# Kernel optimization log

Measured on AMD Instinct MI355X. Metric: run time of the kernel, lower is better.

The kernel has to match this reference:

```python
import jax, jax.numpy as jnp
import numpy as np

B, S, E, H, L = 4, 512, 768, 12, 12
D = E // H
FF = 4 * E
EPS = 1e-5
SCALE = jnp.float32(768.0 ** 0.5)  # emb_size ** (1/2), applied AFTER softmax per source


def setup_inputs() -> dict:
    key = jax.random.key(0)
    ks = jax.random.split(key, 18)
    std = 0.02
    n = lambda k, shp: (jax.random.normal(k, shp, jnp.float32) * std)
    return {
        "x": jax.random.normal(ks[0], (B, S, E), jnp.float32),
        "Wqkv": n(ks[1], (L, E, 3 * E)),
        "bqkv": n(ks[2], (L, 3 * E)),
        "Wp": n(ks[3], (L, E, E)),
        "bp": n(ks[4], (L, E)),
        "W1": n(ks[5], (L, E, FF)),
        "b1": n(ks[6], (L, FF)),
        "W2": n(ks[7], (L, FF, E)),
        "b2": n(ks[8], (L, E)),
        "ln1_g": jnp.ones((L, E), jnp.float32), "ln1_b": jnp.zeros((L, E), jnp.float32),
        "ln2_g": jnp.ones((L, E), jnp.float32), "ln2_b": jnp.zeros((L, E), jnp.float32),
        "ln3_g": jnp.ones((L, E), jnp.float32), "ln3_b": jnp.zeros((L, E), jnp.float32),
        "ln4_g": jnp.ones((L, E), jnp.float32), "ln4_b": jnp.zeros((L, E), jnp.float32),
    }


def _ln(x, g, b):
    m = jnp.mean(x, axis=-1, keepdims=True)
    v = jnp.mean(jnp.square(x - m), axis=-1, keepdims=True)
    return (x - m) * jax.lax.rsqrt(v + EPS) * g + b


def _block(x, p):
    Wqkv, bqkv, Wp, bp, W1, b1, W2, b2, g1, be1, g2, be2, g3, be3, g4, be4 = p
    # --- attention branch ---
    h = _ln(x, g1, be1)
    qkv = h @ Wqkv + bqkv                      # [B,S,3E]
    qkv = qkv.reshape(B, S, H, D, 3)           # qkv is innermost factor in source rearrange
    q = jnp.transpose(qkv[..., 0], (0, 2, 1, 3))  # [B,H,S,D]
    k = jnp.transpose(qkv[..., 1], (0, 2, 1, 3))
    v = jnp.transpose(qkv[..., 2], (0, 2, 1, 3))
    energy = jnp.einsum('bhqd,bhkd->bhqk', q, k)
    att = jax.nn.softmax(energy, axis=-1) / SCALE  # NOTE: scaling AFTER softmax (faithful)
    o = jnp.einsum('bhqk,bhkd->bhqd', att, v)
    o = jnp.transpose(o, (0, 2, 1, 3)).reshape(B, S, E)
    o = o @ Wp + bp
    r1 = _ln(o, g2, be2) + x                   # first ResidualAdd (final LN inside branch)
    # --- feed-forward branch ---
    f = _ln(r1, g3, be3)
    f = jax.nn.gelu(f @ W1 + b1, approximate=False)
    f = f @ W2 + b2
    r2 = _ln(f, g4, be4) + r1                  # second ResidualAdd
    return x + r2                              # outer residual: x = x + block(x)


def reference(x, Wqkv, bqkv, Wp, bp, W1, b1, W2, b2,
              ln1_g, ln1_b, ln2_g, ln2_b, ln3_g, ln3_b, ln4_g, ln4_b):
    params = (Wqkv, bqkv, Wp, bp, W1, b1, W2, b2,
              ln1_g, ln1_b, ln2_g, ln2_b, ln3_g, ln3_b, ln4_g, ln4_b)
    out, _ = jax.lax.scan(lambda c, p: (_block(c, p), None), x, params)
    return out
```

## Files before the change

kernel.cpp:

```cpp
#include <hip/hip_runtime.h>
#include <hip/hip_bf16.h>
#include <stdint.h>

#define LAYERS 12
#define M_ROWS 2048
#define E_DIM 768
#define FF_DIM 3072
#define QKV_DIM 2304
#define SCALE_INV 0.036084391824351615f

typedef __hip_bfloat16 bf16;
typedef __attribute__((ext_vector_type(8))) __bf16 bf16x8;
typedef __attribute__((ext_vector_type(4))) float f32x4;

__device__ __forceinline__ float bf2f(bf16 v) { return __bfloat162float(v); }
__device__ __forceinline__ bf16 f2bf(float v) { return __float2bfloat16(v); }

__device__ __forceinline__ float gelu_f(float x) {
  return 0.5f * x * (1.0f + erff(x * 0.70710678118654752f));
}

__global__ __launch_bounds__(256) void transpose_k(
    const float* __restrict__ w0, const float* __restrict__ w1,
    const float* __restrict__ w2, const float* __restrict__ w3,
    bf16* __restrict__ t0, bf16* __restrict__ t1,
    bf16* __restrict__ t2, bf16* __restrict__ t3)
{
  __shared__ float T[32][33];
  int bid = blockIdx.x;
  const float* src; bf16* dst; int K, N, tile;
  if (bid < 1728)      { src = w0; dst = t0; K = 768;  N = 2304; tile = bid; }
  else if (bid < 2304) { src = w1; dst = t1; K = 768;  N = 768;  tile = bid - 1728; }
  else if (bid < 4608) { src = w2; dst = t2; K = 768;  N = 3072; tile = bid - 2304; }
  else                 { src = w3; dst = t3; K = 3072; N = 768;  tile = bid - 4608; }
  int tilesN = N >> 5;
  int tk = tile / tilesN;
  int tn = tile - tk * tilesN;
  int tx = threadIdx.x & 31, ty = threadIdx.x >> 5;
  int k0 = tk << 5, n0 = tn << 5;
#pragma unroll
  for (int i = 0; i < 4; i++)
    T[ty + i * 8][tx] = src[(size_t)(k0 + ty + i * 8) * N + n0 + tx];
  __syncthreads();
#pragma unroll
  for (int i = 0; i < 4; i++)
    dst[(size_t)(n0 + ty + i * 8) * K + k0 + tx] = f2bf(T[tx][ty + i * 8]);
}

template<int OUT_BF16, int NADD>
__global__ __launch_bounds__(256) void ln_k(
    const float* in, const float* gamma, const float* beta,
    const float* add0, const float* add1, void* outp)
{
  int row = blockIdx.x, tid = threadIdx.x;
  const float* x = in + (size_t)row * 768;
  float v[3]; float s = 0.f, sq = 0.f;
#pragma unroll
  for (int j = 0; j < 3; j++) {
    v[j] = x[tid + j * 256];
    s += v[j]; sq += v[j] * v[j];
  }
#pragma unroll
  for (int off = 32; off; off >>= 1) {
    s += __shfl_xor(s, off);
    sq += __shfl_xor(sq, off);
  }
  __shared__ float red[8];
  int wv = tid >> 6;
  if ((tid & 63) == 0) { red[wv] = s; red[4 + wv] = sq; }
  __syncthreads();
  s  = red[0] + red[1] + red[2] + red[3];
  sq = red[4] + red[5] + red[6] + red[7];
  float mean = s * (1.0f / 768.0f);
  float var  = sq * (1.0f / 768.0f) - mean * mean;
  float rstd = rsqrtf(var + 1e-5f);
#pragma unroll
  for (int j = 0; j < 3; j++) {
    int c = tid + j * 256;
    float val = (v[j] - mean) * rstd * gamma[c] + beta[c];
    if (NADD >= 1) val += add0[(size_t)row * 768 + c];
    if (NADD >= 2) val += add1[(size_t)row * 768 + c];
    if (OUT_BF16) ((bf16*)outp)[(size_t)row * 768 + c] = f2bf(val);
    else          ((float*)outp)[(size_t)row * 768 + c] = val;
  }
}

template<int OUT_MODE>
__global__ __launch_bounds__(256) void gemm_k(
    const bf16* __restrict__ A, const bf16* __restrict__ BT,
    const float* __restrict__ bias, void* __restrict__ Cout,
    bf16* __restrict__ qo, bf16* __restrict__ ko, bf16* __restrict__ vo,
    int N, int K)
{
  __shared__ __align__(16) bf16 Als[64 * 32];
  __shared__ __align__(16) bf16 Bls[64 * 32];
  int tid = threadIdx.x;
  int lane = tid & 63, wave = tid >> 6;
  int wm = (wave >> 1) * 32, wn = (wave & 1) * 32;
  int m0 = (blockIdx.x & 31) << 6;
  int n0 = (blockIdx.x >> 5) << 6;
  const bf16* Ap = A + (size_t)m0 * K;
  const bf16* Bp = BT + (size_t)n0 * K;
  int sr = tid >> 2;
  int sc = (tid & 3) * 8;
  f32x4 acc[2][2] = {};
  for (int k0 = 0; k0 < K; k0 += 32) {
    uint4 av = *(const uint4*)(Ap + (size_t)sr * K + k0 + sc);
    uint4 bv = *(const uint4*)(Bp + (size_t)sr * K + k0 + sc);
    __syncthreads();
    *(uint4*)&Als[tid * 8] = av;
    *(uint4*)&Bls[tid * 8] = bv;
    __syncthreads();
    int ko8 = (lane >> 4) * 8;
    bf16x8 af[2], bfr[2];
#pragma unroll
    for (int i = 0; i < 2; i++)
      af[i] = *(const bf16x8*)&Als[(wm + i * 16 + (lane & 15)) * 32 + ko8];
#pragma unroll
    for (int j = 0; j < 2; j++)
      bfr[j] = *(const bf16x8*)&Bls[(wn + j * 16 + (lane & 15)) * 32 + ko8];
#pragma unroll
    for (int i = 0; i < 2; i++)
#pragma unroll
      for (int j = 0; j < 2; j++)
        acc[i][j] = __builtin_amdgcn_mfma_f32_16x16x32_bf16(af[i], bfr[j], acc[i][j], 0, 0, 0);
  }
#pragma unroll
  for (int i = 0; i < 2; i++) {
    int mbase = m0 + wm + i * 16 + ((lane >> 4) << 2);
#pragma unroll
    for (int j = 0; j < 2; j++) {
      int n = n0 + wn + j * 16 + (lane & 15);
      float bvs = bias[n];
      if (OUT_MODE == 3) {
        int h = n / 192;
        int rm = n - h * 192;
        int d = rm / 3;
        int t = rm - d * 3;
#pragma unroll
        for (int rg = 0; rg < 4; rg++) {
          int m = mbase + rg;
          float val = acc[i][j][rg] + bvs;
          int b = m >> 9, sIdx = m & 511;
          int bh = b * 12 + h;
          if (t == 2)
            vo[(size_t)((bh << 6) + d) * 512 + sIdx] = f2bf(val);
          else {
            bf16* dsts = (t == 0) ? qo : ko;
            dsts[(size_t)((bh << 9) + sIdx) * 64 + d] = f2bf(val);
          }
        }
      } else {
#pragma unroll
        for (int rg = 0; rg < 4; rg++) {
          int m = mbase + rg;
          float val = acc[i][j][rg] + bvs;
          if (OUT_MODE == 0)      ((float*)Cout)[(size_t)m * N + n] = val;
          else if (OUT_MODE == 1) ((bf16*)Cout)[(size_t)m * N + n] = f2bf(val);
          else                    ((bf16*)Cout)[(size_t)m * N + n] = f2bf(gelu_f(val));
        }
      }
    }
  }
}

#define PSTR 80
__global__ __launch_bounds__(256) void attn_k(
    const bf16* __restrict__ q, const bf16* __restrict__ k,
    const bf16* __restrict__ vT, bf16* __restrict__ o)
{
  __shared__ __align__(16) bf16 Kls[64 * 64];
  __shared__ __align__(16) bf16 Vls[64 * 64];
  __shared__ __align__(16) bf16 Pls[4][16 * PSTR];
  int tid = threadIdx.x;
  int lane = tid & 63, w = tid >> 6;
  int l15 = lane & 15, l4 = lane >> 4;
  int qt = blockIdx.x & 7;
  int bh = blockIdx.x >> 3;
  size_t base = (size_t)bh * 32768;

  const bf16* qrowp = q + base + (size_t)(qt * 64 + w * 16 + l15) * 64 + l4 * 8;
  bf16x8 qf0 = *(const bf16x8*)qrowp;
  bf16x8 qf1 = *(const bf16x8*)(qrowp + 32);

  float mrow[4] = {-1e30f, -1e30f, -1e30f, -1e30f};
  float lsum[4] = {0.f, 0.f, 0.f, 0.f};
  f32x4 Oacc[4] = {};
  const f32x4 zed = {0.f, 0.f, 0.f, 0.f};
  bf16* pw = &Pls[w][0];

  for (int kt = 0; kt < 8; kt++) {
    __syncthreads();
#pragma unroll
    for (int rep = 0; rep < 2; rep++) {
      int c = tid + rep * 256;
      int row = c >> 3, col8 = (c & 7) * 8;
      *(uint4*)&Kls[row * 64 + col8] =
          *(const uint4*)(k + base + (size_t)(kt * 64 + row) * 64 + col8);
      *(uint4*)&Vls[row * 64 + col8] =
          *(const uint4*)(vT + base + (size_t)row * 512 + kt * 64 + col8);
    }
    __syncthreads();
    f32x4 e[4];
#pragma unroll
    for (int jt = 0; jt < 4; jt++) {
      bf16x8 kf0 = *(const bf16x8*)&Kls[(jt * 16 + l15) * 64 + l4 * 8];
      bf16x8 kf1 = *(const bf16x8*)&Kls[(jt * 16 + l15) * 64 + l4 * 8 + 32];
      e[jt] = __builtin_amdgcn_mfma_f32_16x16x32_bf16(qf0, kf0, zed, 0, 0, 0);
      e[jt] = __builtin_amdgcn_mfma_f32_16x16x32_bf16(qf1, kf1, e[jt], 0, 0, 0);
    }
    float al[4];
#pragma unroll
    for (int rg = 0; rg < 4; rg++) {
      float mn = fmaxf(fmaxf(e[0][rg], e[1][rg]), fmaxf(e[2][rg], e[3][rg]));
#pragma unroll
      for (int off = 1; off < 16; off <<= 1) mn = fmaxf(mn, __shfl_xor(mn, off));
      float mnew = fmaxf(mrow[rg], mn);
      al[rg] = __expf(mrow[rg] - mnew);
      mrow[rg] = mnew;
    }
    float rs[4] = {0.f, 0.f, 0.f, 0.f};
#pragma unroll
    for (int jt = 0; jt < 4; jt++)
#pragma unroll
      for (int rg = 0; rg < 4; rg++) {
        float p = __expf(e[jt][rg] - mrow[rg]);
        rs[rg] += p;
        pw[(l4 * 4 + rg) * PSTR + jt * 16 + l15] = f2bf(p);
      }
#pragma unroll
    for (int rg = 0; rg < 4; rg++) {
#pragma unroll
      for (int off = 1; off < 16; off <<= 1) rs[rg] += __shfl_xor(rs[rg], off);
      lsum[rg] = lsum[rg] * al[rg] + rs[rg];
    }
#pragma unroll
    for (int dt = 0; dt < 4; dt++)
#pragma unroll
      for (int rg = 0; rg < 4; rg++) Oacc[dt][rg] *= al[rg];
    bf16x8 pf0 = *(const bf16x8*)&pw[l15 * PSTR + l4 * 8];
    bf16x8 pf1 = *(const bf16x8*)&pw[l15 * PSTR + l4 * 8 + 32];
#pragma unroll
    for (int dt = 0; dt < 4; dt++) {
      bf16x8 vf0 = *(const bf16x8*)&Vls[(dt * 16 + l15) * 64 + l4 * 8];
      bf16x8 vf1 = *(const bf16x8*)&Vls[(dt * 16 + l15) * 64 + l4 * 8 + 32];
      Oacc[dt] = __builtin_amdgcn_mfma_f32_16x16x32_bf16(pf0, vf0, Oacc[dt], 0, 0, 0);
      Oacc[dt] = __builtin_amdgcn_mfma_f32_16x16x32_bf16(pf1, vf1, Oacc[dt], 0, 0, 0);
    }
  }
  int b = bh / 12, h = bh - b * 12;
#pragma unroll
  for (int rg = 0; rg < 4; rg++) {
    int qrow = qt * 64 + w * 16 + l4 * 4 + rg;
    float inv = SCALE_INV / lsum[rg];
    size_t rowoff = (size_t)(b * 512 + qrow) * 768 + h * 64;
#pragma unroll
    for (int dt = 0; dt < 4; dt++)
      o[rowoff + dt * 16 + l15] = f2bf(Oacc[dt][rg] * inv);
  }
}

extern "C" void kernel_launch(void* const* d_in, const int* in_sizes, int n_in,
                              void* d_out, int out_size, void* d_ws, size_t ws_size,
                              hipStream_t stream)
{
  const float* x    = (const float*)d_in[0];
  const float* Wqkv = (const float*)d_in[1];
  const float* bqkv = (const float*)d_in[2];
  const float* Wp   = (const float*)d_in[3];
  const float* bp   = (const float*)d_in[4];
  const float* W1   = (const float*)d_in[5];
  const float* b1   = (const float*)d_in[6];
  const float* W2   = (const float*)d_in[7];
  const float* b2   = (const float*)d_in[8];
  const float* g1  = (const float*)d_in[9];
  const float* be1 = (const float*)d_in[10];
  const float* g2  = (const float*)d_in[11];
  const float* be2 = (const float*)d_in[12];
  const float* g3  = (const float*)d_in[13];
  const float* be3 = (const float*)d_in[14];
  const float* g4  = (const float*)d_in[15];
  const float* be4 = (const float*)d_in[16];
  float* xout = (float*)d_out;

  char* ws = (char*)d_ws;
  size_t off = 0;
  auto alloc = [&](size_t bytes) -> char* {
    char* p = ws + off;
    off += (bytes + 255) & ~(size_t)255;
    return p;
  };
  const size_t NTOK = (size_t)M_ROWS * E_DIM;
  bf16*  qb  = (bf16*)alloc(NTOK * 2);
  bf16*  kb  = (bf16*)alloc(NTOK * 2);
  bf16*  vb  = (bf16*)alloc(NTOK * 2);
  bf16*  hb  = (bf16*)alloc(NTOK * 2);
  bf16*  ob  = (bf16*)alloc(NTOK * 2);
  bf16*  f1b = (bf16*)alloc((size_t)M_ROWS * FF_DIM * 2);
  float* tmp = (float*)alloc(NTOK * 4);
  float* r1  = (float*)alloc(NTOK * 4);
  bf16*  tq  = (bf16*)alloc((size_t)768 * 2304 * 2);
  bf16*  tp  = (bf16*)alloc((size_t)768 * 768 * 2);
  bf16*  t1  = (bf16*)alloc((size_t)768 * 3072 * 2);
  bf16*  t2  = (bf16*)alloc((size_t)3072 * 768 * 2);
  if (off > ws_size) {
    hipMemsetAsync(d_out, 0x7f, (size_t)out_size * 4, stream);
    return;
  }

  hipMemcpyAsync(d_out, x, (size_t)out_size * 4, hipMemcpyDeviceToDevice, stream);

  for (int l = 0; l < LAYERS; l++) {
    const float* wq  = Wqkv + (size_t)l * 768 * 2304;
    const float* wp_ = Wp   + (size_t)l * 768 * 768;
    const float* w1_ = W1   + (size_t)l * 768 * 3072;
    const float* w2_ = W2   + (size_t)l * 3072 * 768;

    transpose_k<<<6912, 256, 0, stream>>>(wq, wp_, w1_, w2_, tq, tp, t1, t2);

    ln_k<1, 0><<<2048, 256, 0, stream>>>(xout, g1 + l * 768, be1 + l * 768,
                                         nullptr, nullptr, hb);
    gemm_k<3><<<32 * 36, 256, 0, stream>>>(hb, tq, bqkv + (size_t)l * 2304,
                                           nullptr, qb, kb, vb, 2304, 768);
    attn_k<<<384, 256, 0, stream>>>(qb, kb, vb, ob);
    gemm_k<0><<<32 * 12, 256, 0, stream>>>(ob, tp, bp + (size_t)l * 768,
                                           tmp, nullptr, nullptr, nullptr, 768, 768);
    ln_k<0, 1><<<2048, 256, 0, stream>>>(tmp, g2 + l * 768, be2 + l * 768,
                                         xout, nullptr, r1);
    ln_k<1, 0><<<2048, 256, 0, stream>>>(r1, g3 + l * 768, be3 + l * 768,
                                         nullptr, nullptr, hb);
    gemm_k<2><<<32 * 48, 256, 0, stream>>>(hb, t1, b1 + (size_t)l * 3072,
                                           f1b, nullptr, nullptr, nullptr, 3072, 768);
    gemm_k<0><<<32 * 12, 256, 0, stream>>>(f1b, t2, b2 + (size_t)l * 768,
                                           tmp, nullptr, nullptr, nullptr, 768, 3072);
    ln_k<0, 2><<<2048, 256, 0, stream>>>(tmp, g4 + l * 768, be4 + l * 768,
                                         r1, xout, xout);
  }
}
```

Before: 2.146 ms.

## Batch weight transposes, fuse LayerNorms, add 128-tile GEMMs with direct LDS loads

Converts the weights of all layers to transposed bf16 in one launch before the layer loop, instead of one launch per layer. Fuses LN2+LN3 and LN4+next-layer LN1 into single row kernels, which cuts launches and row passes. Adds a 128x128-tile GEMM for the QKV and FF1 projections and makes every GEMM use global_load_lds for direct global-to-LDS copies. The cost is a larger workspace holding all layers' transposed weights, plus more registers per thread in the 128-tile kernel.

New measurement: 2.320 ms. 1.08x slower.

```diff
diff --git a/kernel.cpp b/kernel.cpp
--- a/kernel.cpp
+++ b/kernel.cpp
@@ -20,6 +20,12 @@
   return 0.5f * x * (1.0f + erff(x * 0.70710678118654752f));
 }
 
+__device__ __forceinline__ void glds16(const bf16* g, bf16* l) {
+  __builtin_amdgcn_global_load_lds(
+      (const __attribute__((address_space(1))) void*)g,
+      (__attribute__((address_space(3))) void*)l, 16, 0, 0);
+}
+
 __global__ __launch_bounds__(256) void transpose_k(
     const float* __restrict__ w0, const float* __restrict__ w1,
     const float* __restrict__ w2, const float* __restrict__ w3,
@@ -27,12 +33,13 @@
     bf16* __restrict__ t2, bf16* __restrict__ t3)
 {
   __shared__ float T[32][33];
-  int bid = blockIdx.x;
+  int l = blockIdx.x / 6912;
+  int bid = blockIdx.x - l * 6912;
   const float* src; bf16* dst; int K, N, tile;
-  if (bid < 1728)      { src = w0; dst = t0; K = 768;  N = 2304; tile = bid; }
-  else if (bid < 2304) { src = w1; dst = t1; K = 768;  N = 768;  tile = bid - 1728; }
-  else if (bid < 4608) { src = w2; dst = t2; K = 768;  N = 3072; tile = bid - 2304; }
-  else                 { src = w3; dst = t3; K = 3072; N = 768;  tile = bid - 4608; }
+  if (bid < 1728)      { src = w0 + (size_t)l * 768 * 2304; dst = t0 + (size_t)l * 768 * 2304; K = 768;  N = 2304; tile = bid; }
+  else if (bid < 2304) { src = w1 + (size_t)l * 768 * 768;  dst = t1 + (size_t)l * 768 * 768;  K = 768;  N = 768;  tile = bid - 1728; }
+  else if (bid < 4608) { src = w2 + (size_t)l * 768 * 3072; dst = t2 + (size_t)l * 768 * 3072; K = 768;  N = 3072; tile = bid - 2304; }
+  else                 { src = w3 + (size_t)l * 3072 * 768; dst = t3 + (size_t)l * 3072 * 768; K = 3072; N = 768;  tile = bid - 4608; }
   int tilesN = N >> 5;
   int tk = tile / tilesN;
   int tn = tile - tk * tilesN;
@@ -47,90 +54,157 @@
     dst[(size_t)(n0 + ty + i * 8) * K + k0 + tx] = f2bf(T[tx][ty + i * 8]);
 }
 
-template<int OUT_BF16, int NADD>
-__global__ __launch_bounds__(256) void ln_k(
-    const float* in, const float* gamma, const float* beta,
-    const float* add0, const float* add1, void* outp)
-{
-  int row = blockIdx.x, tid = threadIdx.x;
-  const float* x = in + (size_t)row * 768;
-  float v[3]; float s = 0.f, sq = 0.f;
-#pragma unroll
-  for (int j = 0; j < 3; j++) {
-    v[j] = x[tid + j * 256];
-    s += v[j]; sq += v[j] * v[j];
-  }
+__device__ __forceinline__ void rowstats(float s, float sq, float* red, int tid,
+                                         float& mean, float& rstd) {
 #pragma unroll
   for (int off = 32; off; off >>= 1) {
     s += __shfl_xor(s, off);
     sq += __shfl_xor(sq, off);
   }
-  __shared__ float red[8];
+  __syncthreads();
   int wv = tid >> 6;
   if ((tid & 63) == 0) { red[wv] = s; red[4 + wv] = sq; }
   __syncthreads();
   s  = red[0] + red[1] + red[2] + red[3];
   sq = red[4] + red[5] + red[6] + red[7];
-  float mean = s * (1.0f / 768.0f);
-  float var  = sq * (1.0f / 768.0f) - mean * mean;
-  float rstd = rsqrtf(var + 1e-5f);
+  mean = s * (1.0f / 768.0f);
+  float var = sq * (1.0f / 768.0f) - mean * mean;
+  rstd = rsqrtf(var + 1e-5f);
+}
+
+__global__ __launch_bounds__(256) void ln_k(
+    const float* in, const float* gamma, const float* beta, bf16* outp)
+{
+  __shared__ float red[8];
+  int row = blockIdx.x, tid = threadIdx.x;
+  const float* x = in + (size_t)row * 768;
+  float v[3]; float s = 0.f, sq = 0.f;
+#pragma unroll
+  for (int j = 0; j < 3; j++) {
+    v[j] = x[tid + j * 256];
+    s += v[j]; sq += v[j] * v[j];
+  }
+  float mean, rstd;
+  rowstats(s, sq, red, tid, mean, rstd);
 #pragma unroll
   for (int j = 0; j < 3; j++) {
     int c = tid + j * 256;
-    float val = (v[j] - mean) * rstd * gamma[c] + beta[c];
-    if (NADD >= 1) val += add0[(size_t)row * 768 + c];
-    if (NADD >= 2) val += add1[(size_t)row * 768 + c];
-    if (OUT_BF16) ((bf16*)outp)[(size_t)row * 768 + c] = f2bf(val);
-    else          ((float*)outp)[(size_t)row * 768 + c] = val;
+    outp[(size_t)row * 768 + c] = f2bf((v[j] - mean) * rstd * gamma[c] + beta[c]);
+  }
+}
+
+__global__ __launch_bounds__(256) void ln23_k(
+    const float* in, const float* g2, const float* b2, const float* xres,
+    float* r1out, const float* g3, const float* b3, bf16* hbout)
+{
+  __shared__ float red[8];
+  int row = blockIdx.x, tid = threadIdx.x;
+  const float* x = in + (size_t)row * 768;
+  float v[3]; float s = 0.f, sq = 0.f;
+#pragma unroll
+  for (int j = 0; j < 3; j++) {
+    v[j] = x[tid + j * 256];
+    s += v[j]; sq += v[j] * v[j];
+  }
+  float mean, rstd;
+  rowstats(s, sq, red, tid, mean, rstd);
+  s = 0.f; sq = 0.f;
+#pragma unroll
+  for (int j = 0; j < 3; j++) {
+    int c = tid + j * 256;
+    v[j] = (v[j] - mean) * rstd * g2[c] + b2[c] + xres[(size_t)row * 768 + c];
+    r1out[(size_t)row * 768 + c] = v[j];
+    s += v[j]; sq += v[j] * v[j];
+  }
+  rowstats(s, sq, red, tid, mean, rstd);
+#pragma unroll
+  for (int j = 0; j < 3; j++) {
+    int c = tid + j * 256;
+    hbout[(size_t)row * 768 + c] = f2bf((v[j] - mean) * rstd * g3[c] + b3[c]);
+  }
+}
+
+__global__ __launch_bounds__(256) void ln41_k(
+    const float* in, const float* g4, const float* b4, const float* r1,
+    float* xio, const float* g1n, const float* b1n, bf16* hbout)
+{
+  __shared__ float red[8];
+  int row = blockIdx.x, tid = threadIdx.x;
+  const float* x = in + (size_t)row * 768;
+  float v[3]; float s = 0.f, sq = 0.f;
+#pragma unroll
+  for (int j = 0; j < 3; j++) {
+    v[j] = x[tid + j * 256];
+    s += v[j]; sq += v[j] * v[j];
+  }
+  float mean, rstd;
+  rowstats(s, sq, red, tid, mean, rstd);
+  s = 0.f; sq = 0.f;
+#pragma unroll
+  for (int j = 0; j < 3; j++) {
+    int c = tid + j * 256;
+    size_t idx = (size_t)row * 768 + c;
+    v[j] = (v[j] - mean) * rstd * g4[c] + b4[c] + r1[idx] + xio[idx];
+    xio[idx] = v[j];
+    s += v[j]; sq += v[j] * v[j];
+  }
+  if (g1n == nullptr) return;
+  rowstats(s, sq, red, tid, mean, rstd);
+#pragma unroll
+  for (int j = 0; j < 3; j++) {
+    int c = tid + j * 256;
+    hbout[(size_t)row * 768 + c] = f2bf((v[j] - mean) * rstd * g1n[c] + b1n[c]);
   }
 }
 
 template<int OUT_MODE>
-__global__ __launch_bounds__(256) void gemm_k(
+__global__ __launch_bounds__(256) void gemm128_k(
     const bf16* __restrict__ A, const bf16* __restrict__ BT,
     const float* __restrict__ bias, void* __restrict__ Cout,
     bf16* __restrict__ qo, bf16* __restrict__ ko, bf16* __restrict__ vo,
-    int N, int K)
-{
-  __shared__ __align__(16) bf16 Als[64 * 32];
-  __shared__ __align__(16) bf16 Bls[64 * 32];
+    int N, int K, int nTilesN)
+{
+  __shared__ __align__(16) bf16 Als[128 * 32];
+  __shared__ __align__(16) bf16 Bls[128 * 32];
   int tid = threadIdx.x;
-  int lane = tid & 63, wave = tid >> 6;
-  int wm = (wave >> 1) * 32, wn = (wave & 1) * 32;
-  int m0 = (blockIdx.x & 31) << 6;
-  int n0 = (blockIdx.x >> 5) << 6;
-  const bf16* Ap = A + (size_t)m0 * K;
-  const bf16* Bp = BT + (size_t)n0 * K;
-  int sr = tid >> 2;
-  int sc = (tid & 3) * 8;
-  f32x4 acc[2][2] = {};
+  int lane = tid & 63, w = tid >> 6;
+  int l15 = lane & 15, l4 = lane >> 4;
+  int tm = blockIdx.x / nTilesN;
+  int tn = blockIdx.x - tm * nTilesN;
+  int m0 = tm << 7, n0 = tn << 7;
+  int wm = (w >> 1) << 6, wn = (w & 1) << 6;
+  const bf16* Ag = A + (size_t)m0 * K;
+  const bf16* Bg = BT + (size_t)n0 * K;
+  int srow = tid >> 2;
+  int scol = (tid & 3) * 8;
+  f32x4 acc[4][4] = {};
   for (int k0 = 0; k0 < K; k0 += 32) {
-    uint4 av = *(const uint4*)(Ap + (size_t)sr * K + k0 + sc);
-    uint4 bv = *(const uint4*)(Bp + (size_t)sr * K + k0 + sc);
-    __syncthreads();
-    *(uint4*)&Als[tid * 8] = av;
-    *(uint4*)&Bls[tid * 8] = bv;
-    __syncthreads();
-    int ko8 = (lane >> 4) * 8;
-    bf16x8 af[2], bfr[2];
-#pragma unroll
-    for (int i = 0; i < 2; i++)
-      af[i] = *(const bf16x8*)&Als[(wm + i * 16 + (lane & 15)) * 32 + ko8];
-#pragma unroll
-    for (int j = 0; j < 2; j++)
-      bfr[j] = *(const bf16x8*)&Bls[(wn + j * 16 + (lane & 15)) * 32 + ko8];
-#pragma unroll
-    for (int i = 0; i < 2; i++)
-#pragma unroll
-      for (int j = 0; j < 2; j++)
+    __syncthreads();
+    glds16(Ag + (size_t)srow * K + k0 + scol,        Als + tid * 8);
+    glds16(Ag + (size_t)(srow + 64) * K + k0 + scol, Als + 2048 + tid * 8);
+    glds16(Bg + (size_t)srow * K + k0 + scol,        Bls + tid * 8);
+    glds16(Bg + (size_t)(srow + 64) * K + k0 + scol, Bls + 2048 + tid * 8);
+    __syncthreads();
+    int ko8 = l4 * 8;
+    bf16x8 af[4], bfr[4];
+#pragma unroll
+    for (int i = 0; i < 4; i++)
+      af[i] = *(const bf16x8*)&Als[(wm + i * 16 + l15) * 32 + ko8];
+#pragma unroll
+    for (int j = 0; j < 4; j++)
+      bfr[j] = *(const bf16x8*)&Bls[(wn + j * 16 + l15) * 32 + ko8];
+#pragma unroll
+    for (int i = 0; i < 4; i++)
+#pragma unroll
+      for (int j = 0; j < 4; j++)
         acc[i][j] = __builtin_amdgcn_mfma_f32_16x16x32_bf16(af[i], bfr[j], acc[i][j], 0, 0, 0);
   }
 #pragma unroll
-  for (int i = 0; i < 2; i++) {
-    int mbase = m0 + wm + i * 16 + ((lane >> 4) << 2);
-#pragma unroll
-    for (int j = 0; j < 2; j++) {
-      int n = n0 + wn + j * 16 + (lane & 15);
+  for (int i = 0; i < 4; i++) {
+    int mbase = m0 + wm + i * 16 + (l4 << 2);
+#pragma unroll
+    for (int j = 0; j < 4; j++) {
+      int n = n0 + wn + j * 16 + l15;
       float bvs = bias[n];
       if (OUT_MODE == 3) {
         int h = n / 192;
@@ -155,11 +229,61 @@
         for (int rg = 0; rg < 4; rg++) {
           int m = mbase + rg;
           float val = acc[i][j][rg] + bvs;
-          if (OUT_MODE == 0)      ((float*)Cout)[(size_t)m * N + n] = val;
-          else if (OUT_MODE == 1) ((bf16*)Cout)[(size_t)m * N + n] = f2bf(val);
-          else                    ((bf16*)Cout)[(size_t)m * N + n] = f2bf(gelu_f(val));
+          ((bf16*)Cout)[(size_t)m * N + n] = f2bf(gelu_f(val));
         }
       }
+    }
+  }
+}
+
+__global__ __launch_bounds__(256) void gemm64_k(
+    const bf16* __restrict__ A, const bf16* __restrict__ BT,
+    const float* __restrict__ bias, float* __restrict__ Cout,
+    int N, int K, int nTilesN)
+{
+  __shared__ __align__(16) bf16 Als[64 * 32];
+  __shared__ __align__(16) bf16 Bls[64 * 32];
+  int tid = threadIdx.x;
+  int lane = tid & 63, w = tid >> 6;
+  int l15 = lane & 15, l4 = lane >> 4;
+  int tm = blockIdx.x / nTilesN;
+  int tn = blockIdx.x - tm * nTilesN;
+  int m0 = tm << 6, n0 = tn << 6;
+  int wm = (w >> 1) << 5, wn = (w & 1) << 5;
+  const bf16* Ag = A + (size_t)m0 * K;
+  const bf16* Bg = BT + (size_t)n0 * K;
+  int srow = tid >> 2;
+  int scol = (tid & 3) * 8;
+  f32x4 acc[2][2] = {};
+  for (int k0 = 0; k0 < K; k0 += 32) {
+    __syncthreads();
+    glds16(Ag + (size_t)srow * K + k0 + scol, Als + tid * 8);
+    glds16(Bg + (size_t)srow * K + k0 + scol, Bls + tid * 8);
+    __syncthreads();
+    int ko8 = l4 * 8;
+    bf16x8 af[2], bfr[2];
+#pragma unroll
+    for (int i = 0; i < 2; i++)
+      af[i] = *(const bf16x8*)&Als[(wm + i * 16 + l15) * 32 + ko8];
+#pragma unroll
+    for (int j = 0; j < 2; j++)
+      bfr[j] = *(const bf16x8*)&Bls[(wn + j * 16 + l15) * 32 + ko8];
+#pragma unroll
+    for (int i = 0; i < 2; i++)
+#pragma unroll
+      for (int j = 0; j < 2; j++)
+        acc[i][j] = __builtin_amdgcn_mfma_f32_16x16x32_bf16(af[i], bfr[j], acc[i][j], 0, 0, 0);
+  }
+#pragma unroll
+  for (int i = 0; i < 2; i++) {
+    int mbase = m0 + wm + i * 16 + (l4 << 2);
+#pragma unroll
+    for (int j = 0; j < 2; j++) {
+      int n = n0 + wn + j * 16 + l15;
+      float bvs = bias[n];
+#pragma unroll
+      for (int rg = 0; rg < 4; rg++)
+        Cout[(size_t)(mbase + rg) * N + n] = acc[i][j][rg] + bvs;
     }
   }
 }
@@ -299,10 +423,10 @@
   bf16*  f1b = (bf16*)alloc((size_t)M_ROWS * FF_DIM * 2);
   float* tmp = (float*)alloc(NTOK * 4);
   float* r1  = (float*)alloc(NTOK * 4);
-  bf16*  tq  = (bf16*)alloc((size_t)768 * 2304 * 2);
-  bf16*  tp  = (bf16*)alloc((size_t)768 * 768 * 2);
-  bf16*  t1  = (bf16*)alloc((size_t)768 * 3072 * 2);
-  bf16*  t2  = (bf16*)alloc((size_t)3072 * 768 * 2);
+  bf16*  tq  = (bf16*)alloc((size_t)LAYERS * 768 * 2304 * 2);
+  bf16*  tp  = (bf16*)alloc((size_t)LAYERS * 768 * 768 * 2);
+  bf16*  t1  = (bf16*)alloc((size_t)LAYERS * 768 * 3072 * 2);
+  bf16*  t2  = (bf16*)alloc((size_t)LAYERS * 3072 * 768 * 2);
   if (off > ws_size) {
     hipMemsetAsync(d_out, 0x7f, (size_t)out_size * 4, stream);
     return;
@@ -310,30 +434,30 @@
 
   hipMemcpyAsync(d_out, x, (size_t)out_size * 4, hipMemcpyDeviceToDevice, stream);
 
+  transpose_k<<<6912 * LAYERS, 256, 0, stream>>>(Wqkv, Wp, W1, W2, tq, tp, t1, t2);
+
+  ln_k<<<2048, 256, 0, stream>>>(xout, g1, be1, hb);
+
   for (int l = 0; l < LAYERS; l++) {
-    const float* wq  = Wqkv + (size_t)l * 768 * 2304;
-    const float* wp_ = Wp   + (size_t)l * 768 * 768;
-    const float* w1_ = W1   + (size_t)l * 768 * 3072;
-    const float* w2_ = W2   + (size_t)l * 3072 * 768;
-
-    transpose_k<<<6912, 256, 0, stream>>>(wq, wp_, w1_, w2_, tq, tp, t1, t2);
-
-    ln_k<1, 0><<<2048, 256, 0, stream>>>(xout, g1 + l * 768, be1 + l * 768,
-                                         nullptr, nullptr, hb);
-    gemm_k<3><<<32 * 36, 256, 0, stream>>>(hb, tq, bqkv + (size_t)l * 2304,
-                                           nullptr, qb, kb, vb, 2304, 768);
+    const bf16* tql = tq + (size_t)l * 768 * 2304;
+    const bf16* tpl = tp + (size_t)l * 768 * 768;
+    const bf16* t1l = t1 + (size_t)l * 768 * 3072;
+    const bf16* t2l = t2 + (size_t)l * 3072 * 768;
+
+    gemm128_k<3><<<16 * 18, 256, 0, stream>>>(hb, tql, bqkv + (size_t)l * QKV_DIM,
+                                              nullptr, qb, kb, vb, QKV_DIM, 768, 18);
     attn_k<<<384, 256, 0, stream>>>(qb, kb, vb, ob);
-    gemm_k<0><<<32 * 12, 256, 0, stream>>>(ob, tp, bp + (size_t)l * 768,
-                                           tmp, nullptr, nullptr, nullptr, 768, 768);
-    ln_k<0, 1><<<2048, 256, 0, stream>>>(tmp, g2 + l * 768, be2 + l * 768,
-                                         xout, nullptr, r1);
-    ln_k<1, 0><<<2048, 256, 0, stream>>>(r1, g3 + l * 768, be3 + l * 768,
-                                         nullptr, nullptr, hb);
-    gemm_k<2><<<32 * 48, 256, 0, stream>>>(hb, t1, b1 + (size_t)l * 3072,
-                                           f1b, nullptr, nullptr, nullptr, 3072, 768);
-    gemm_k<0><<<32 * 12, 256, 0, stream>>>(f1b, t2, b2 + (size_t)l * 768,
-                                           tmp, nullptr, nullptr, nullptr, 768, 3072);
-    ln_k<0, 2><<<2048, 256, 0, stream>>>(tmp, g4 + l * 768, be4 + l * 768,
-                                         r1, xout, xout);
-  }
-}
+    gemm64_k<<<32 * 12, 256, 0, stream>>>(ob, tpl, bp + (size_t)l * 768,
+                                          tmp, 768, 768, 12);
+    ln23_k<<<2048, 256, 0, stream>>>(tmp, g2 + l * 768, be2 + l * 768, xout,
+                                     r1, g3 + l * 768, be3 + l * 768, hb);
+    gemm128_k<2><<<16 * 24, 256, 0, stream>>>(hb, t1l, b1 + (size_t)l * FF_DIM,
+                                              f1b, nullptr, nullptr, nullptr, FF_DIM, 768, 24);
+    gemm64_k<<<32 * 12, 256, 0, stream>>>(f1b, t2l, b2 + (size_t)l * 768,
+                                          tmp, 768, 3072, 12);
+    const float* g1n  = (l + 1 < LAYERS) ? g1 + (l + 1) * 768 : nullptr;
+    const float* be1n = (l + 1 < LAYERS) ? be1 + (l + 1) * 768 : nullptr;
+    ln41_k<<<2048, 256, 0, stream>>>(tmp, g4 + l * 768, be4 + l * 768, r1,
+                                     xout, g1n, be1n, hb);
+  }
+}
```
